# Kernel tuning notes

Hardware: AMD Instinct MI355X
Metric: run time of the kernel (lower is better)

## Reference

```python
import jax, jax.numpy as jnp
import numpy as np

N_GROUPS = 32
EPS = 1e-5


def group_norm(x, gamma, beta):
    b, c, h, w = x.shape
    xg = x.reshape(b, N_GROUPS, c // N_GROUPS, h, w)
    mean = xg.mean(axis=(2, 3, 4), keepdims=True)
    var = xg.var(axis=(2, 3, 4), keepdims=True)
    xn = ((xg - mean) * jax.lax.rsqrt(var + EPS)).reshape(b, c, h, w)
    return xn * gamma[None, :, None, None] + beta[None, :, None, None]


def conv1x1(x, W, b):
    # x: [b,c,h,w], W: [out,in], b: [out]
    return jnp.einsum('bchw,oc->bohw', x, W) + b[None, :, None, None]


def setup_inputs() -> dict:
    key = jax.random.key(0)
    ks = jax.random.split(key, 6)
    B, C, H, W = 8, 256, 64, 64
    s = 1.0 / np.sqrt(C)
    return {
        'x': jax.random.normal(ks[0], (B, C, H, W), dtype=jnp.float32),
        'norm_gamma': jnp.ones((C,), jnp.float32),
        'norm_beta': jnp.zeros((C,), jnp.float32),
        'Wq': jax.random.normal(ks[1], (C, C), jnp.float32) * s,
        'bq': jnp.zeros((C,), jnp.float32),
        'Wk': jax.random.normal(ks[2], (C, C), jnp.float32) * s,
        'bk': jnp.zeros((C,), jnp.float32),
        'Wv': jax.random.normal(ks[3], (C, C), jnp.float32) * s,
        'bv': jnp.zeros((C,), jnp.float32),
        'Wo': jax.random.normal(ks[4], (C, C), jnp.float32) * s,
        'bo': jnp.zeros((C,), jnp.float32),
    }


def reference(x, norm_gamma, norm_beta, Wq, bq, Wk, bk, Wv, bv, Wo, bo):
    b, c, h, w = x.shape
    hn = group_norm(x, norm_gamma, norm_beta)
    q = conv1x1(hn, Wq, bq).reshape(b, c, h * w)  # [b,c,hw]
    k = conv1x1(hn, Wk, bk).reshape(b, c, h * w)
    v = conv1x1(hn, Wv, bv).reshape(b, c, h * w)
    # scores[b,i,j] = sum_c q[b,c,i] * k[b,c,j]; scale is int(c)*-0.5
    # (faithful to the source, which multiplies by -0.5*c, NOT c**-0.5)
    scores = jnp.einsum('bci,bcj->bij', q, k) * (c * -0.5)
    attn = jax.nn.softmax(scores, axis=2)  # softmax over j (keys)
    # h_[b,c,i] = sum_j v[b,c,j] * attn[b,i,j]
    h_ = jnp.einsum('bcj,bij->bci', v, attn).reshape(b, c, h, w)
    # source applies self.out to the ORIGINAL input x and adds attention output
    return h_ + conv1x1(x, Wo, bo)
```

## Files before the change

### kernel.cpp

```cpp
#include <hip/hip_runtime.h>
#include <hip/hip_bf16.h>


typedef __attribute__((ext_vector_type(8))) short bf16x8;
typedef __attribute__((ext_vector_type(4))) short s16x4;
typedef __attribute__((ext_vector_type(8))) short s16x8;
typedef __attribute__((ext_vector_type(4))) float f32x4;

#define MFMA16(a, b, c) __builtin_amdgcn_mfma_f32_16x16x32_bf16((a), (b), (c), 0, 0, 0)

#define SCALE_Q (-184.66496523378734f)

__device__ __forceinline__ short f2bf(float f) {
  unsigned int u = __builtin_bit_cast(unsigned int, f);
  u = (u + 0x7FFFu + ((u >> 16) & 1u)) >> 16;
  return (short)(unsigned short)u;
}
__device__ __forceinline__ short t2bf(float f) {
  return (short)(__builtin_bit_cast(unsigned int, f) >> 16);
}
__device__ __forceinline__ float bf2f(short h) {
  unsigned int u = ((unsigned int)(unsigned short)h) << 16;
  return __builtin_bit_cast(float, u);
}
__device__ __forceinline__ void async16(void* lds, const void* g) {
  __builtin_amdgcn_global_load_lds(
      (const __attribute__((address_space(1))) unsigned int*)g,
      (__attribute__((address_space(3))) unsigned int*)lds, 16, 0, 0);
}
__device__ __forceinline__ void lgkm_barrier() {
  asm volatile("s_waitcnt lgkmcnt(0)" ::: "memory");
  __builtin_amdgcn_s_barrier();
  __builtin_amdgcn_sched_barrier(0);
}

__global__ void wsplit_k(const float* __restrict__ Wq, const float* __restrict__ Wk,
                         const float* __restrict__ Wv, const float* __restrict__ Wo,
                         short* __restrict__ whi, short* __restrict__ wlo) {
  int idx = blockIdx.x * 256 + threadIdx.x;
  int m = idx >> 16;
  int e = idx & 65535;
  const float* W = (m == 0) ? Wq : (m == 1) ? Wk : (m == 2) ? Wv : Wo;
  float v = W[e];
  short h = f2bf(v);
  whi[idx] = h;
  wlo[idx] = f2bf(v - bf2f(h));
}

__global__ __launch_bounds__(256) void gn_fused_k(
    const float* __restrict__ x, const float* __restrict__ gamma,
    const float* __restrict__ beta, short* __restrict__ hn_hi,
    short* __restrict__ hn_lo) {
  int b = blockIdx.x, g = blockIdx.y, tid = threadIdx.x;
  const float* p = x + ((size_t)(b * 32 + g)) * 32768;
  float s = 0.f, sq = 0.f;
  for (int it = 0; it < 32; ++it) {
    f32x4 v = *(const f32x4*)(p + (size_t)(it * 256 + tid) * 4);
    s += v[0] + v[1] + v[2] + v[3];
    sq += v[0] * v[0] + v[1] * v[1] + v[2] * v[2] + v[3] * v[3];
  }
#pragma unroll
  for (int off = 1; off < 64; off <<= 1) {
    s += __shfl_xor(s, off);
    sq += __shfl_xor(sq, off);
  }
  __shared__ float ls[4], lq[4];
  if ((tid & 63) == 0) { ls[tid >> 6] = s; lq[tid >> 6] = sq; }
  __syncthreads();
  float S = ls[0] + ls[1] + ls[2] + ls[3];
  float Q = lq[0] + lq[1] + lq[2] + lq[3];
  float mean = S * (1.f / 32768.f);
  float rstd = rsqrtf(Q * (1.f / 32768.f) - mean * mean + 1e-5f);
  int c0 = g * 8;
  float ga[8], be[8];
#pragma unroll
  for (int cc = 0; cc < 8; ++cc) {
    ga[cc] = gamma[c0 + cc] * rstd;
    be[cc] = beta[c0 + cc] - mean * ga[cc];
  }
  for (int it = 0; it < 16; ++it) {
    int i = it * 256 + tid;
    s16x8 hv, lv;
#pragma unroll
    for (int cc = 0; cc < 8; ++cc) {
      float xv = p[(size_t)cc * 4096 + i];
      float h = xv * ga[cc] + be[cc];
      short hh = f2bf(h);
      hv[cc] = hh;
      lv[cc] = f2bf(h - bf2f(hh));
    }
    size_t ro = ((size_t)(b * 4096 + i)) * 256 + c0;
    *(s16x8*)(hn_hi + ro) = hv;
    *(s16x8*)(hn_lo + ro) = lv;
  }
}

__global__ __launch_bounds__(256) void proj_qk_k(
    const short* __restrict__ hn_hi, const short* __restrict__ hn_lo,
    const short* __restrict__ whi, const short* __restrict__ wlo,
    const float* __restrict__ bq, const float* __restrict__ bk,
    short* __restrict__ q_hi, short* __restrict__ q_lo,
    short* __restrict__ k_hi, short* __restrict__ k_lo) {
  int tid = threadIdx.x, w = tid >> 6, lane = tid & 63, l4 = lane & 15, g = lane >> 4;
  int iblk = blockIdx.x, y = blockIdx.y, b = blockIdx.z;
  const short* wh = whi + y * 65536;
  const short* wl = wlo + y * 65536;
  const float* bias = y ? bk : bq;
  short* ohi = (y ? k_hi : q_hi) + (size_t)b * 1048576;
  short* olo = (y ? k_lo : q_lo) + (size_t)b * 1048576;
  float scale = y ? 1.0f : SCALE_Q;
  int arow = iblk * 64 + w * 16 + l4;
  const short* ha = hn_hi + ((size_t)(b * 4096 + arow)) * 256 + g * 8;
  const short* la = hn_lo + ((size_t)(b * 4096 + arow)) * 256 + g * 8;
  f32x4 acc[16];
#pragma unroll
  for (int i = 0; i < 16; ++i) acc[i] = (f32x4){0.f, 0.f, 0.f, 0.f};
  for (int ks = 0; ks < 8; ++ks) {
    bf16x8 ah = *(const bf16x8*)(ha + ks * 32);
    bf16x8 al = *(const bf16x8*)(la + ks * 32);
#pragma unroll
    for (int ct = 0; ct < 16; ++ct) {
      bf16x8 bh = *(const bf16x8*)(wh + (ct * 16 + l4) * 256 + ks * 32 + g * 8);
      bf16x8 bl = *(const bf16x8*)(wl + (ct * 16 + l4) * 256 + ks * 32 + g * 8);
      acc[ct] = MFMA16(ah, bh, acc[ct]);
      acc[ct] = MFMA16(al, bh, acc[ct]);
      acc[ct] = MFMA16(ah, bl, acc[ct]);
    }
  }
  int orow = iblk * 64 + w * 16 + g * 4;
#pragma unroll
  for (int ct = 0; ct < 16; ++ct) {
    int c = ct * 16 + l4;
    float bsv = bias[c];
#pragma unroll
    for (int r = 0; r < 4; ++r) {
      float val = (acc[ct][r] + bsv) * scale;
      short h = f2bf(val);
      short lo = f2bf(val - bf2f(h));
      size_t off = ((size_t)(orow + r)) * 256 + c;
      ohi[off] = h;
      olo[off] = lo;
    }
  }
}

__global__ __launch_bounds__(256) void proj_v_k(
    const short* __restrict__ hn_hi, const short* __restrict__ wv_hi,
    const float* __restrict__ bv, short* __restrict__ vout) {
  int tid = threadIdx.x, w = tid >> 6, lane = tid & 63, l4 = lane & 15, g = lane >> 4;
  int jblk = blockIdx.x, cblk = blockIdx.y, b = blockIdx.z;
  int crow = cblk * 64 + w * 16 + l4;
  const short* ap = wv_hi + (size_t)crow * 256 + g * 8;
  f32x4 acc[4];
#pragma unroll
  for (int i = 0; i < 4; ++i) acc[i] = (f32x4){0.f, 0.f, 0.f, 0.f};
  for (int ks = 0; ks < 8; ++ks) {
    bf16x8 a = *(const bf16x8*)(ap + ks * 32);
#pragma unroll
    for (int jt = 0; jt < 4; ++jt) {
      bf16x8 bb = *(const bf16x8*)(hn_hi +
          ((size_t)(b * 4096 + jblk * 64 + jt * 16 + l4)) * 256 + ks * 32 + g * 8);
      acc[jt] = MFMA16(a, bb, acc[jt]);
    }
  }
#pragma unroll
  for (int jt = 0; jt < 4; ++jt) {
#pragma unroll
    for (int r = 0; r < 4; ++r) {
      int c = cblk * 64 + w * 16 + g * 4 + r;
      int j = jblk * 64 + jt * 16 + l4;
      float val = acc[jt][r] + bv[c];
      vout[((size_t)(b * 256 + c)) * 4096 + j] = f2bf(val);
    }
  }
}

__global__ __launch_bounds__(256, 2) void flash3b_k(
    const short* __restrict__ qhi, const short* __restrict__ qlo,
    const short* __restrict__ khi, const short* __restrict__ klo,
    const short* __restrict__ vv, const float* __restrict__ x,
    const short* __restrict__ wo_hi, const float* __restrict__ bo,
    float* __restrict__ out) {
  __shared__ short k_hi_s[2][8192];
  __shared__ short k_lo_s[2][8192];
  __shared__ short p_s[2048];
  __shared__ __attribute__((aligned(16))) float albuf[64];
  __shared__ __attribute__((aligned(16))) float flagbuf[4];
  __shared__ __attribute__((aligned(16))) float lsmbuf[64];

  int tid = threadIdx.x, w = tid >> 6, lane = tid & 63, l4 = lane & 15, g = lane >> 4;
  int b = blockIdx.x, i0 = blockIdx.y * 64;
  size_t boff = (size_t)b * 1048576;
  const short* qh_p = qhi + boff;
  const short* ql_p = qlo + boff;
  const char* kh_g = (const char*)(khi + boff);
  const char* kl_g = (const char*)(klo + boff);
  const short* v_p = vv + boff;

  int qrow = i0 + w * 16 + l4;
  bf16x8 qh[8], ql[8];
#pragma unroll
  for (int ks = 0; ks < 8; ++ks) {
    qh[ks] = *(const bf16x8*)(qh_p + (size_t)qrow * 256 + ks * 32 + g * 8);
    ql[ks] = *(const bf16x8*)(ql_p + (size_t)qrow * 256 + ks * 32 + g * 8);
  }

  f32x4 oac[4][4];
#pragma unroll
  for (int it = 0; it < 4; ++it)
#pragma unroll
    for (int ct = 0; ct < 4; ++ct) oac[it][ct] = (f32x4){0.f, 0.f, 0.f, 0.f};
  float m_cur = -1e30f, lsum = 0.f;

  int sx = (l4 & 7) << 4;
  int colx[8];
#pragma unroll
  for (int ks = 0; ks < 8; ++ks) colx[ks] = (ks * 64 + g * 16) ^ sx;
  int krow_b = l4 * 512;

  int ksrc[4];
#pragma unroll
  for (int it = 0; it < 4; ++it) {
    int d = tid * 16 + it * 4096;
    int krow = d >> 9, kcol = d & 511;
    ksrc[it] = krow * 512 + (kcol ^ ((krow & 7) << 4));
  }

  char* khs = (char*)k_hi_s;
  char* kls = (char*)k_lo_s;
  char* ps = (char*)p_s;
  int cbase = w * 64;
  bf16x8 vreg[4];

#pragma unroll
  for (int it = 0; it < 4; ++it) {
    int ldst = w * 1024 + it * 4096;
    async16(khs + ldst, kh_g + ksrc[it]);
    async16(kls + ldst, kl_g + ksrc[it]);
  }

  for (int js = 0; js < 128; ++js) {
    int cur = (js & 1) * 16384;
    __syncthreads();
#pragma unroll
    for (int ct = 0; ct < 4; ++ct)
      vreg[ct] = *(const bf16x8*)(v_p + (size_t)(cbase + ct * 16 + l4) * 4096 +
                                  js * 32 + g * 8);
    if (js < 127) {
      int kgo = (js + 1) * 16384;
      int nxt = ((js + 1) & 1) * 16384;
#pragma unroll
      for (int it = 0; it < 4; ++it) {
        int ldst = nxt + w * 1024 + it * 4096;
        async16(khs + ldst, kh_g + kgo + ksrc[it]);
        async16(kls + ldst, kl_g + kgo + ksrc[it]);
      }
    }

    f32x4 st0 = (f32x4){0.f, 0.f, 0.f, 0.f};
    f32x4 st1 = (f32x4){0.f, 0.f, 0.f, 0.f};
    __builtin_amdgcn_s_setprio(1);
#pragma unroll
    for (int ks = 0; ks < 8; ++ks) {
      bf16x8 kh0 = *(const bf16x8*)(khs + cur + krow_b + colx[ks]);
      bf16x8 kh1 = *(const bf16x8*)(khs + cur + krow_b + colx[ks] + 8192);
      bf16x8 kl0 = *(const bf16x8*)(kls + cur + krow_b + colx[ks]);
      bf16x8 kl1 = *(const bf16x8*)(kls + cur + krow_b + colx[ks] + 8192);
      st0 = MFMA16(kh0, qh[ks], st0);
      st1 = MFMA16(kh1, qh[ks], st1);
      st0 = MFMA16(kl0, qh[ks], st0);
      st1 = MFMA16(kl1, qh[ks], st1);
      st0 = MFMA16(kh0, ql[ks], st0);
      st1 = MFMA16(kh1, ql[ks], st1);
    }
    __builtin_amdgcn_s_setprio(0);

    float pmax = fmaxf(fmaxf(fmaxf(st0[0], st0[1]), fmaxf(st0[2], st0[3])),
                       fmaxf(fmaxf(st1[0], st1[1]), fmaxf(st1[2], st1[3])));
    pmax = fmaxf(pmax, __shfl_xor(pmax, 16));
    pmax = fmaxf(pmax, __shfl_xor(pmax, 32));
    float alpha = 1.0f;
    bool upd = !__all(pmax <= m_cur + 11.0f);
    if (upd) {
      float m_new = fmaxf(m_cur, pmax);
      alpha = exp2f(m_cur - m_new);
      lsum *= alpha;
      m_cur = m_new;
    }
    f32x4 e0, e1;
#pragma unroll
    for (int r = 0; r < 4; ++r) {
      e0[r] = exp2f(st0[r] - m_cur);
      e1[r] = exp2f(st1[r] - m_cur);
    }
    float lps = e0[0] + e0[1] + e0[2] + e0[3] + e1[0] + e1[1] + e1[2] + e1[3];
    lps += __shfl_xor(lps, 16);
    lps += __shfl_xor(lps, 32);
    lsum += lps;

    s16x4 pw0 = {t2bf(e0[0]), t2bf(e0[1]), t2bf(e0[2]), t2bf(e0[3])};
    s16x4 pw1 = {t2bf(e1[0]), t2bf(e1[1]), t2bf(e1[2]), t2bf(e1[3])};
    int wb = (w * 16 + l4) * 64 + g * 8;
    *(s16x4*)(ps + wb) = pw0;
    *(s16x4*)(ps + wb + 32) = pw1;
    if (lane < 16) albuf[w * 16 + lane] = alpha;
    if (lane == 0) flagbuf[w] = upd ? 1.f : 0.f;

    lgkm_barrier();

    f32x4 fl = *(const f32x4*)(&flagbuf[0]);
    if (fl[0] + fl[1] + fl[2] + fl[3] > 0.f) {
#pragma unroll
      for (int it = 0; it < 4; ++it) {
        f32x4 av = *(const f32x4*)(&albuf[it * 16 + g * 4]);
#pragma unroll
        for (int ct = 0; ct < 4; ++ct)
#pragma unroll
          for (int r = 0; r < 4; ++r) oac[it][ct][r] *= av[r];
      }
    }
    __builtin_amdgcn_s_setprio(1);
#pragma unroll
    for (int it = 0; it < 4; ++it) {
      bf16x8 pf = *(const bf16x8*)(ps + (it * 16 + l4) * 64 + g * 16);
#pragma unroll
      for (int ct = 0; ct < 4; ++ct) oac[it][ct] = MFMA16(pf, vreg[ct], oac[it][ct]);
    }
    __builtin_amdgcn_s_setprio(0);
  }

  if (lane < 16) lsmbuf[w * 16 + lane] = lsum;
  __syncthreads();
#pragma unroll
  for (int it = 0; it < 4; ++it) {
    f32x4 lv = *(const f32x4*)(&lsmbuf[it * 16 + g * 4]);
    f32x4 iv = {1.f / lv[0], 1.f / lv[1], 1.f / lv[2], 1.f / lv[3]};
#pragma unroll
    for (int ct = 0; ct < 4; ++ct)
#pragma unroll
      for (int r = 0; r < 4; ++r) oac[it][ct][r] *= iv[r];
  }
  const float* xb = x + (size_t)b * 1048576;
  for (int ks = 0; ks < 8; ++ks) {
    bf16x8 af[4], bfr[4];
#pragma unroll
    for (int it = 0; it < 4; ++it) {
#pragma unroll
      for (int e = 0; e < 8; ++e) {
        float xv = xb[(size_t)(ks * 32 + g * 8 + e) * 4096 + i0 + it * 16 + l4];
        af[it][e] = t2bf(xv);
      }
    }
#pragma unroll
    for (int ct = 0; ct < 4; ++ct)
      bfr[ct] = *(const bf16x8*)(wo_hi + (cbase + ct * 16 + l4) * 256 + ks * 32 + g * 8);
#pragma unroll
    for (int it = 0; it < 4; ++it)
#pragma unroll
      for (int ct = 0; ct < 4; ++ct) oac[it][ct] = MFMA16(af[it], bfr[ct], oac[it][ct]);
  }
  float* ob = out + (size_t)b * 1048576;
#pragma unroll
  for (int ct = 0; ct < 4; ++ct) {
    float bov = bo[cbase + ct * 16 + l4];
#pragma unroll
    for (int it = 0; it < 4; ++it) {
      float* ad = ob + (size_t)(cbase + ct * 16 + l4) * 4096 + i0 + it * 16 + g * 4;
      f32x4 res;
#pragma unroll
      for (int r = 0; r < 4; ++r) res[r] = oac[it][ct][r] + bov;
      *(f32x4*)ad = res;
    }
  }
}

extern "C" void kernel_launch(void* const* d_in, const int* in_sizes, int n_in,
                              void* d_out, int out_size, void* d_ws, size_t ws_size,
                              hipStream_t stream) {
  (void)in_sizes; (void)n_in; (void)out_size; (void)ws_size;
  const float* x = (const float*)d_in[0];
  const float* gamma = (const float*)d_in[1];
  const float* beta = (const float*)d_in[2];
  const float* Wq = (const float*)d_in[3];
  const float* bq = (const float*)d_in[4];
  const float* Wk = (const float*)d_in[5];
  const float* bk = (const float*)d_in[6];
  const float* Wv = (const float*)d_in[7];
  const float* bv = (const float*)d_in[8];
  const float* Wo = (const float*)d_in[9];
  const float* bo = (const float*)d_in[10];
  float* out = (float*)d_out;
  char* ws = (char*)d_ws;

  const size_t MB16 = 16777216;
  short* whi = (short*)(ws + 4096);
  short* wlo = (short*)(ws + 4096 + 524288);
  char* base = ws + 4096 + 2 * 524288;
  short* hnhi = (short*)(base);
  short* hnlo = (short*)(base + MB16);
  short* qhi = (short*)(base + 2 * MB16);
  short* qlo = (short*)(base + 3 * MB16);
  short* khi = (short*)(base + 4 * MB16);
  short* klo = (short*)(base + 5 * MB16);
  short* vvp = (short*)(base + 6 * MB16);

  wsplit_k<<<dim3(1024), dim3(256), 0, stream>>>(Wq, Wk, Wv, Wo, whi, wlo);
  gn_fused_k<<<dim3(8, 32), dim3(256), 0, stream>>>(x, gamma, beta, hnhi, hnlo);
  proj_qk_k<<<dim3(64, 2, 8), dim3(256), 0, stream>>>(hnhi, hnlo, whi, wlo, bq, bk,
                                                      qhi, qlo, khi, klo);
  proj_v_k<<<dim3(64, 4, 8), dim3(256), 0, stream>>>(hnhi, whi + 2 * 65536, bv, vvp);
  flash3b_k<<<dim3(8, 64), dim3(256), 0, stream>>>(qhi, qlo, khi, klo, vvp, x,
                                                   whi + 3 * 65536, bo, out);
}
```

Before: 537.9 us.

## Replace async LDS double buffer with register-staged single-buffer K prefetch

The flash kernel drops the double-buffered direct-to-LDS async K loads. It now prefetches the next K tile into registers at the top of each iteration and writes it to a single LDS buffer after the PV MFMAs. This halves K LDS usage and raises the launch-bounds occupancy hint to 3 blocks per CU. In exchange it adds register pressure and VGPR-to-LDS store traffic, and a tighter register cap could cause spills.

```diff
diff --git a/kernel.cpp b/kernel.cpp
--- a/kernel.cpp
+++ b/kernel.cpp
@@ -22,11 +22,6 @@
 __device__ __forceinline__ float bf2f(short h) {
   unsigned int u = ((unsigned int)(unsigned short)h) << 16;
   return __builtin_bit_cast(float, u);
-}
-__device__ __forceinline__ void async16(void* lds, const void* g) {
-  __builtin_amdgcn_global_load_lds(
-      (const __attribute__((address_space(1))) unsigned int*)g,
-      (__attribute__((address_space(3))) unsigned int*)lds, 16, 0, 0);
 }
 __device__ __forceinline__ void lgkm_barrier() {
   asm volatile("s_waitcnt lgkmcnt(0)" ::: "memory");
@@ -175,14 +170,14 @@
   }
 }
 
-__global__ __launch_bounds__(256, 2) void flash3b_k(
+__global__ __launch_bounds__(256, 3) void flash7_k(
     const short* __restrict__ qhi, const short* __restrict__ qlo,
     const short* __restrict__ khi, const short* __restrict__ klo,
     const short* __restrict__ vv, const float* __restrict__ x,
     const short* __restrict__ wo_hi, const float* __restrict__ bo,
     float* __restrict__ out) {
-  __shared__ short k_hi_s[2][8192];
-  __shared__ short k_lo_s[2][8192];
+  __shared__ short k_hi_s[8192];
+  __shared__ short k_lo_s[8192];
   __shared__ short p_s[2048];
   __shared__ __attribute__((aligned(16))) float albuf[64];
   __shared__ __attribute__((aligned(16))) float flagbuf[4];
@@ -218,54 +213,56 @@
   for (int ks = 0; ks < 8; ++ks) colx[ks] = (ks * 64 + g * 16) ^ sx;
   int krow_b = l4 * 512;
 
-  int ksrc[4];
+  int glin[4], ldst[4];
 #pragma unroll
   for (int it = 0; it < 4; ++it) {
     int d = tid * 16 + it * 4096;
+    glin[it] = d;
     int krow = d >> 9, kcol = d & 511;
-    ksrc[it] = krow * 512 + (kcol ^ ((krow & 7) << 4));
+    ldst[it] = krow * 512 + (kcol ^ ((krow & 7) << 4));
   }
 
   char* khs = (char*)k_hi_s;
   char* kls = (char*)k_lo_s;
   char* ps = (char*)p_s;
   int cbase = w * 64;
-  bf16x8 vreg[4];
+  bf16x8 vreg[4], krh[4], krl[4];
 
 #pragma unroll
   for (int it = 0; it < 4; ++it) {
-    int ldst = w * 1024 + it * 4096;
-    async16(khs + ldst, kh_g + ksrc[it]);
-    async16(kls + ldst, kl_g + ksrc[it]);
+    krh[it] = *(const bf16x8*)(kh_g + glin[it]);
+    krl[it] = *(const bf16x8*)(kl_g + glin[it]);
+  }
+#pragma unroll
+  for (int it = 0; it < 4; ++it) {
+    *(bf16x8*)(khs + ldst[it]) = krh[it];
+    *(bf16x8*)(kls + ldst[it]) = krl[it];
   }
 
   for (int js = 0; js < 128; ++js) {
-    int cur = (js & 1) * 16384;
     __syncthreads();
+    if (js < 127) {
+      int kgo = (js + 1) * 16384;
+#pragma unroll
+      for (int it = 0; it < 4; ++it) {
+        krh[it] = *(const bf16x8*)(kh_g + kgo + glin[it]);
+        krl[it] = *(const bf16x8*)(kl_g + kgo + glin[it]);
+      }
+    }
 #pragma unroll
     for (int ct = 0; ct < 4; ++ct)
       vreg[ct] = *(const bf16x8*)(v_p + (size_t)(cbase + ct * 16 + l4) * 4096 +
                                   js * 32 + g * 8);
-    if (js < 127) {
-      int kgo = (js + 1) * 16384;
-      int nxt = ((js + 1) & 1) * 16384;
-#pragma unroll
-      for (int it = 0; it < 4; ++it) {
-        int ldst = nxt + w * 1024 + it * 4096;
-        async16(khs + ldst, kh_g + kgo + ksrc[it]);
-        async16(kls + ldst, kl_g + kgo + ksrc[it]);
-      }
-    }
 
     f32x4 st0 = (f32x4){0.f, 0.f, 0.f, 0.f};
     f32x4 st1 = (f32x4){0.f, 0.f, 0.f, 0.f};
     __builtin_amdgcn_s_setprio(1);
 #pragma unroll
     for (int ks = 0; ks < 8; ++ks) {
-      bf16x8 kh0 = *(const bf16x8*)(khs + cur + krow_b + colx[ks]);
-      bf16x8 kh1 = *(const bf16x8*)(khs + cur + krow_b + colx[ks] + 8192);
-      bf16x8 kl0 = *(const bf16x8*)(kls + cur + krow_b + colx[ks]);
-      bf16x8 kl1 = *(const bf16x8*)(kls + cur + krow_b + colx[ks] + 8192);
+      bf16x8 kh0 = *(const bf16x8*)(khs + krow_b + colx[ks]);
+      bf16x8 kh1 = *(const bf16x8*)(khs + krow_b + colx[ks] + 8192);
+      bf16x8 kl0 = *(const bf16x8*)(kls + krow_b + colx[ks]);
+      bf16x8 kl1 = *(const bf16x8*)(kls + krow_b + colx[ks] + 8192);
       st0 = MFMA16(kh0, qh[ks], st0);
       st1 = MFMA16(kh1, qh[ks], st1);
       st0 = MFMA16(kl0, qh[ks], st0);
@@ -327,6 +324,14 @@
       for (int ct = 0; ct < 4; ++ct) oac[it][ct] = MFMA16(pf, vreg[ct], oac[it][ct]);
     }
     __builtin_amdgcn_s_setprio(0);
+
+    if (js < 127) {
+#pragma unroll
+      for (int it = 0; it < 4; ++it) {
+        *(bf16x8*)(khs + ldst[it]) = krh[it];
+        *(bf16x8*)(kls + ldst[it]) = krl[it];
+      }
+    }
   }
 
   if (lane < 16) lsmbuf[w * 16 + lane] = lsum;
@@ -340,7 +345,7 @@
 #pragma unroll
       for (int r = 0; r < 4; ++r) oac[it][ct][r] *= iv[r];
   }
-  const float* xb = x + (size_t)b * 1048576;
+  const float* xb = x + boff;
   for (int ks = 0; ks < 8; ++ks) {
     bf16x8 af[4], bfr[4];
 #pragma unroll
@@ -359,7 +364,7 @@
 #pragma unroll
       for (int ct = 0; ct < 4; ++ct) oac[it][ct] = MFMA16(af[it], bfr[ct], oac[it][ct]);
   }
-  float* ob = out + (size_t)b * 1048576;
+  float* ob = out + boff;
 #pragma unroll
   for (int ct = 0; ct < 4; ++ct) {
     float bov = bo[cbase + ct * 16 + l4];
@@ -409,6 +414,6 @@
   proj_qk_k<<<dim3(64, 2, 8), dim3(256), 0, stream>>>(hnhi, hnlo, whi, wlo, bq, bk,
                                                       qhi, qlo, khi, klo);
   proj_v_k<<<dim3(64, 4, 8), dim3(256), 0, stream>>>(hnhi, whi + 2 * 65536, bv, vvp);
-  flash3b_k<<<dim3(8, 64), dim3(256), 0, stream>>>(qhi, qlo, khi, klo, vvp, x,
-                                                   whi + 3 * 65536, bo, out);
-}
+  flash7_k<<<dim3(8, 64), dim3(256), 0, stream>>>(qhi, qlo, khi, klo, vvp, x,
+                                                  whi + 3 * 65536, bo, out);
+}
```

New measurement: 1.777 ms. +230.3%, slower.
